# Optimization experiments

Measured on AMD Instinct MI355X. Metric: run time of the kernel, lower is better.

## Reference

```python
import jax, jax.numpy as jnp
import numpy as np

K_TOP = 4
NUM_EXPERTS = 8


def _lstm_dir(x, wih, whh, b):
    # x: [B,T,in], wih: [4H,in], whh: [4H,H], b: [4H] (b_ih+b_hh)
    xW = jnp.einsum('bti,gi->btg', x, wih) + b  # [B,T,4H]
    B = x.shape[0]
    H = whh.shape[1]
    init = (jnp.zeros((B, H), x.dtype), jnp.zeros((B, H), x.dtype))

    def step(carry, xt):
        h, c = carry
        g = xt + h @ whh.T
        i, f, gg, o = jnp.split(g, 4, axis=-1)  # torch gate order i,f,g,o
        c = jax.nn.sigmoid(f) * c + jax.nn.sigmoid(i) * jnp.tanh(gg)
        h = jax.nn.sigmoid(o) * jnp.tanh(c)
        return (h, c), h

    _, hs = jax.lax.scan(step, init, jnp.swapaxes(xW, 0, 1))  # [T,B,H]
    return jnp.swapaxes(hs, 0, 1)


def _bidir_layer(x, Wih, Whh, bih, bhh):
    # Wih: [2,4H,in]; dir 0 forward, dir 1 backward
    hf = _lstm_dir(x, Wih[0], Whh[0], bih[0] + bhh[0])
    hb = _lstm_dir(x[:, ::-1], Wih[1], Whh[1], bih[1] + bhh[1])[:, ::-1]
    return jnp.concatenate([hf, hb], axis=-1)  # [B,T,2H]


def _expert(x, Wih0, Whh0, bih0, bhh0, Wih1, Whh1, bih1, bhh1):
    h = _bidir_layer(x, Wih0, Whh0, bih0, bhh0)   # [B,T,2H]
    h = _bidir_layer(h, Wih1, Whh1, bih1, bhh1)   # [B,T,2H]
    return h


def _cv_squared(v):
    v = v.astype(jnp.float32)
    return jnp.var(v, ddof=1) / (jnp.mean(v) ** 2 + 1e-10)


def _forward(x, spk, wg_w, wg_b, Wih0, Whh0, bih0, bhh0, Wih1, Whh1, bih1, bhh1, fc1_w, fc1_b, fc_w, fc_b, loss_coef=0.01):
    B, T, _ = x.shape
    # --- top-k gating (eval path: clean logits, no noise) ---
    logits = spk @ wg_w.T + wg_b                      # [B,E]
    top_vals, top_idx = jax.lax.top_k(logits, K_TOP + 1)
    gates_k = jax.nn.softmax(top_vals[:, :K_TOP], axis=-1)
    rows = jnp.arange(B)[:, None]
    gates = jnp.zeros_like(logits).at[rows, top_idx[:, :K_TOP]].set(gates_k)  # [B,E]
    load = (gates > 0).sum(0)
    importance = gates.sum(0)
    loss = (_cv_squared(importance) + _cv_squared(load)) * loss_coef
    # --- run all experts (dense mixture, as in source) ---
    expert_h = jax.vmap(_expert, in_axes=(None, 0, 0, 0, 0, 0, 0, 0, 0))(
        x, Wih0, Whh0, bih0, bhh0, Wih1, Whh1, bih1, bhh1)          # [E,B,T,2H]
    expert_out = jnp.einsum('ebtf,hf->ebth', expert_h, fc1_w) + fc1_b  # [E,B,T,H]
    data_output = jnp.einsum('ebth,be->bth', expert_out, gates)        # [B,T,H]
    out = jnp.einsum('bth,oh->bto', data_output, fc_w) + fc_b          # [B,T,O]
    out = jnp.swapaxes(out, 0, 1)                                      # [T,B,O]
    return out, loss


def setup_inputs() -> dict:
    key = jax.random.key(0)
    ks = jax.random.split(key, 16)
    B, T, D, H, E, O, S = 32, 1024, 128, 128, 8, 44, 256
    s = 0.08  # weight scale to keep LSTM gates in sane range
    return {
        'x': jax.random.normal(ks[0], (B, T, D), jnp.float32),
        'spk': jax.random.normal(ks[1], (B, S), jnp.float32),
        'wg_w': jax.random.normal(ks[2], (E, S), jnp.float32) * s,
        'wg_b': jax.random.normal(ks[3], (E,), jnp.float32) * s,
        'Wih0': jax.random.normal(ks[4], (E, 2, 4 * H, D), jnp.float32) * s,
        'Whh0': jax.random.normal(ks[5], (E, 2, 4 * H, H), jnp.float32) * s,
        'bih0': jax.random.normal(ks[6], (E, 2, 4 * H), jnp.float32) * s,
        'bhh0': jax.random.normal(ks[7], (E, 2, 4 * H), jnp.float32) * s,
        'Wih1': jax.random.normal(ks[8], (E, 2, 4 * H, 2 * H), jnp.float32) * s,
        'Whh1': jax.random.normal(ks[9], (E, 2, 4 * H, H), jnp.float32) * s,
        'bih1': jax.random.normal(ks[10], (E, 2, 4 * H), jnp.float32) * s,
        'bhh1': jax.random.normal(ks[11], (E, 2, 4 * H), jnp.float32) * s,
        'fc1_w': jax.random.normal(ks[12], (H, 2 * H), jnp.float32) * s,
        'fc1_b': jax.random.normal(ks[13], (H,), jnp.float32) * s,
        'fc_w': jax.random.normal(ks[14], (O, H), jnp.float32) * s,
        'fc_b': jax.random.normal(ks[15], (O,), jnp.float32) * s,
    }


def reference(x, spk, wg_w, wg_b, Wih0, Whh0, bih0, bhh0, Wih1, Whh1, bih1, bhh1, fc1_w, fc1_b, fc_w, fc_b):
    return _forward(x, spk, wg_w, wg_b, Wih0, Whh0, bih0, bhh0, Wih1, Whh1, bih1, bhh1, fc1_w, fc1_b, fc_w, fc_b)
```

## Files before the change

### kernel.cpp

```cpp
#include <hip/hip_runtime.h>

typedef __attribute__((ext_vector_type(4))) float f32x4;
typedef __attribute__((ext_vector_type(8))) short s16x8;

#define LOG2E 1.4426950408889634f
#define K2L   2.8853900817779268f

__device__ __forceinline__ unsigned short f2bf(float f) {
  union { float f; unsigned int i; } v; v.f = f;
  unsigned int u = v.i;
  u = (u + 0x7FFFu + ((u >> 16) & 1u)) >> 16;
  return (unsigned short)u;
}
__device__ __forceinline__ float bf2f(unsigned short s) {
  union { unsigned int i; float f; } v; v.i = ((unsigned int)s) << 16;
  return v.f;
}
__device__ __forceinline__ float rcp_(float x) { return __builtin_amdgcn_rcpf(x); }
__device__ __forceinline__ float ex2(float x) { return __builtin_amdgcn_exp2f(x); }
__device__ __forceinline__ f32x4 mfma16(s16x8 a, s16x8 b, f32x4 c) {
  return __builtin_amdgcn_mfma_f32_16x16x32_bf16(a, b, c, 0, 0, 0);
}
__device__ __forceinline__ s16x8 pack8s(const float* s, float sc) {
  s16x8 v;
#pragma unroll
  for (int j = 0; j < 8; ++j) v[j] = (short)f2bf(s[j] * sc);
  return v;
}

#define OFF_H0   0
#define OFF_XW   134217728
#define OFF_XT   201326592
#define OFF_WHH  209715200
#define OFF_H1C  213909504
#define OFF_HST  230686720
#define OFF_CST  230817792
#define OFF_M    231079936
#define OFF_CV   231129088
#define OFF_G    231129344
#define OFF_WIH0 231130368
#define OFF_WIH1 233227520
#define OFF_BIA  237421824
#define WS_NEED  237552896

__global__ void wsdbg_kernel(float* __restrict__ out, float v) { out[0] = v; }

__global__ void prep_kernel(const float* __restrict__ Whh0, const float* __restrict__ Whh1,
                            const float* __restrict__ Wih0, const float* __restrict__ Wih1,
                            const float* __restrict__ bih0, const float* __restrict__ bhh0,
                            const float* __restrict__ bih1, const float* __restrict__ bhh1,
                            unsigned short* __restrict__ whhb,
                            unsigned short* __restrict__ wihb0,
                            unsigned short* __restrict__ wihb1,
                            float* __restrict__ biasb) {
  const int tid = blockIdx.x * 512 + threadIdx.x;
  for (int i = tid; i < 5242880; i += 2097152) {
    if (i < 2097152) {
      const int gate = (i >> 14) & 3;
      const float sc = (gate == 2) ? K2L : -LOG2E;
      whhb[i] = f2bf((i < 1048576 ? Whh0[i] : Whh1[i - 1048576]) * sc);
    } else if (i < 3145728) {
      const int j = i - 2097152;
      const int gate = (j >> 14) & 3;
      const float sc = (gate == 2) ? K2L : -LOG2E;
      wihb0[j] = f2bf(Wih0[j] * sc);
    } else {
      const int j = i - 3145728;
      const int gate = (j >> 15) & 3;
      const float sc = (gate == 2) ? K2L : -LOG2E;
      wihb1[j] = f2bf(Wih1[j] * sc);
    }
  }
  if (tid < 16384) {
    const int L = tid >> 13, rem = tid & 8191;
    const int gate = (rem >> 7) & 3;
    const float sc = (gate == 2) ? K2L : -LOG2E;
    const float b = L ? (bih1[rem] + bhh1[rem]) : (bih0[rem] + bhh0[rem]);
    biasb[tid] = b * sc;
  }
}

__global__ void prepx_kernel(const float* __restrict__ x, unsigned short* __restrict__ xt) {
  const int i = blockIdx.x * 512 + threadIdx.x;
  for (int j = i; j < 4194304; j += 2097152) {
    const int b = j >> 17, rem = j & 131071, t = rem >> 7, f = rem & 127;
    xt[((size_t)t * 32 + b) * 128 + f] = f2bf(x[j]);
  }
}

__global__ void mprep_kernel(const float* __restrict__ fc1w, const float* __restrict__ fc1b,
                             const float* __restrict__ fcw, const float* __restrict__ fcb,
                             float* __restrict__ M, float* __restrict__ Cv) {
  const int mi = blockIdx.x * 256 + threadIdx.x;
  if (mi < 12288) {
    const int dd = mi / 6144, rem = mi % 6144, o = rem >> 7, hc = rem & 127;
    float s = 0.f;
    if (o < 44)
      for (int h = 0; h < 128; ++h) s += fcw[o * 128 + h] * fc1w[h * 256 + dd * 128 + hc];
    M[mi] = s;
  }
  if (blockIdx.x == 0 && threadIdx.x < 44) {
    const int o = threadIdx.x;
    float s = fcb[o];
    for (int h = 0; h < 128; ++h) s += fcw[o * 128 + h] * fc1b[h];
    Cv[o] = s;
  }
}

__global__ void initout_kernel(const float* __restrict__ Cv, float* __restrict__ out) {
  const int i = blockIdx.x * 512 + threadIdx.x;
  if (i < 1441792) out[i] = Cv[i % 44];
}

__global__ void gating_kernel(const float* __restrict__ spk,
                              const float* __restrict__ wgw,
                              const float* __restrict__ wgb,
                              float* __restrict__ gates_out,
                              float* __restrict__ loss_out) {
  __shared__ __align__(16) float logits[32][8];
  __shared__ __align__(16) float gmat[32][8];
  const int tid = threadIdx.x;
  {
    const int b = tid >> 3, e = tid & 7;
    float s = wgb[e];
    for (int k = 0; k < 256; ++k) s += spk[b * 256 + k] * wgw[e * 256 + k];
    logits[b][e] = s;
  }
  __syncthreads();
  if (tid < 32) {
    const int b = tid;
    float v[8];
    for (int e = 0; e < 8; ++e) v[e] = logits[b][e];
    int idx[4]; float val[4];
    unsigned used = 0;
    for (int k = 0; k < 4; ++k) {
      float best = -1e30f; int bi = 0;
      for (int e = 0; e < 8; ++e)
        if (!((used >> e) & 1) && v[e] > best) { best = v[e]; bi = e; }
      used |= (1u << bi); idx[k] = bi; val[k] = best;
    }
    const float m = val[0];
    float ex[4], ssum = 0.f;
    for (int k = 0; k < 4; ++k) { ex[k] = ex2(LOG2E * (val[k] - m)); ssum += ex[k]; }
    for (int e = 0; e < 8; ++e) gmat[b][e] = 0.f;
    for (int k = 0; k < 4; ++k) gmat[b][idx[k]] = ex[k] / ssum;
    for (int e = 0; e < 8; ++e) gates_out[b * 8 + e] = gmat[b][e];
  }
  __syncthreads();
  if (tid == 0) {
    float imp[8], ld[8];
    for (int e = 0; e < 8; ++e) {
      float si = 0.f, sl = 0.f;
      for (int b = 0; b < 32; ++b) { si += gmat[b][e]; sl += (gmat[b][e] > 0.f) ? 1.f : 0.f; }
      imp[e] = si; ld[e] = sl;
    }
    float mi = 0.f, ml = 0.f;
    for (int e = 0; e < 8; ++e) { mi += imp[e]; ml += ld[e]; }
    mi *= 0.125f; ml *= 0.125f;
    float vi = 0.f, vl = 0.f;
    for (int e = 0; e < 8; ++e) {
      vi += (imp[e] - mi) * (imp[e] - mi);
      vl += (ld[e] - ml) * (ld[e] - ml);
    }
    vi /= 7.f; vl /= 7.f;
    loss_out[0] = 0.01f * (vi / (mi * mi + 1e-10f) + vl / (ml * ml + 1e-10f));
  }
}

template <int L>
__global__ __launch_bounds__(512, 1) void fused(
    int k,
    const unsigned short* __restrict__ Asrc,
    const unsigned short* __restrict__ wihb,
    const float* __restrict__ biasb,
    const unsigned short* __restrict__ whhb,
    unsigned short* __restrict__ xwbufs,
    unsigned short* __restrict__ hstate, float* __restrict__ cstate,
    unsigned short* __restrict__ hout,
    const float* __restrict__ Mmat, const float* __restrict__ gatesp,
    float* __restrict__ outp) {
  constexpr int KC = L ? 8 : 4;
  constexpr int KS = KC * 32;
  const int tid = threadIdx.x, w = tid >> 6, l = tid & 63;
  const int l15 = l & 15, lq = l >> 4;

  if (L && blockIdx.x >= 192) {
    const int c2 = k - 2;
    if (c2 < 0 || c2 > 15) return;
    if (w >= 6) return;
    const int ss = blockIdx.x - 192;
    const int mt = (w >= 3) ? 1 : 0, ot = w - mt * 3;
    const int o = ot * 16 + l15;
    const bool ov = o < 44;
    s16x8 bfm[2][4];
#pragma unroll
    for (int dd = 0; dd < 2; ++dd)
#pragma unroll
      for (int kc = 0; kc < 4; ++kc) {
        if (ov) bfm[dd][kc] = pack8s(Mmat + ((size_t)dd * 48 + o) * 128 + kc * 32 + lq * 8, 1.f);
        else { s16x8 z = {0,0,0,0,0,0,0,0}; bfm[dd][kc] = z; }
      }
    const unsigned short* hb = hout + (size_t)(c2 & 1) * 4194304;
    f32x4 acc0 = {0.f,0.f,0.f,0.f}, acc1 = {0.f,0.f,0.f,0.f};
    for (int e = 0; e < 8; ++e) {
      const unsigned short* ap = hb + ((((size_t)e * 64 + ss) * 32) + mt * 16 + l15) * 256 + lq * 8;
      f32x4 p0 = {0.f,0.f,0.f,0.f}, p1 = {0.f,0.f,0.f,0.f};
#pragma unroll
      for (int kc = 0; kc < 4; ++kc) {
        s16x8 a0 = *(const s16x8*)(ap + kc * 32);
        s16x8 a1 = *(const s16x8*)(ap + 128 + kc * 32);
        p0 = mfma16(a0, bfm[0][kc], p0);
        p1 = mfma16(a1, bfm[1][kc], p1);
      }
#pragma unroll
      for (int r = 0; r < 4; ++r) {
        const float g = gatesp[(mt * 16 + lq * 4 + r) * 8 + e];
        acc0[r] += g * p0[r];
        acc1[r] += g * p1[r];
      }
    }
    if (ov) {
      const int s2 = c2 * 64 + ss, t1 = 1023 - s2;
#pragma unroll
      for (int r = 0; r < 4; ++r) {
        const int b = mt * 16 + lq * 4 + r;
        outp[((size_t)s2 * 32 + b) * 44 + o] += acc0[r];
        outp[((size_t)t1 * 32 + b) * 44 + o] += acc1[r];
      }
    }
    return;
  }

  if (blockIdx.x >= 32) {
    if (k >= 16) return;
    const int gb = blockIdx.x - 32;
    const int ed = gb & 15, e = ed >> 1, d = ed & 1;
    const int slice = gb >> 4;
    const int nsl = L ? 10 : 14;
    unsigned short* xw = xwbufs + (size_t)(k & 1) * 16777216;

    s16x8 bf[4][KC];
    float bias[4];
#pragma unroll
    for (int j = 0; j < 4; ++j) {
      const int n = w * 64 + j * 16 + l15;
      bias[j] = biasb[ed * 512 + n];
      const unsigned short* wp = wihb + ((size_t)ed * 512 + n) * KS + lq * 8;
#pragma unroll
      for (int kc = 0; kc < KC; ++kc) bf[j][kc] = *(const s16x8*)(wp + kc * 32);
    }
    for (int ss = slice; ss < 64; ss += nsl) {
      const int s = k * 64 + ss;
      const int t = d ? 1023 - s : s;
#pragma unroll
      for (int mt = 0; mt < 2; ++mt) {
        const size_t arow = (size_t)(L ? (e * 1024 + t) : t) * 32 + mt * 16 + l15;
        const unsigned short* ap = Asrc + arow * KS + lq * 8;
        s16x8 af[KC];
#pragma unroll
        for (int kc = 0; kc < KC; ++kc) af[kc] = *(const s16x8*)(ap + kc * 32);
        f32x4 acc[4];
#pragma unroll
        for (int j = 0; j < 4; ++j) acc[j] = f32x4{bias[j], bias[j], bias[j], bias[j]};
#pragma unroll
        for (int kc = 0; kc < KC; ++kc) {
#pragma unroll
          for (int j = 0; j < 4; ++j) acc[j] = mfma16(af[kc], bf[j][kc], acc[j]);
        }
        unsigned short* op = xw + (((size_t)(ed * 2 + mt) * 64 + ss) * 512) * 16 + lq * 4;
#pragma unroll
        for (int j = 0; j < 4; ++j) {
          const int n = w * 64 + j * 16 + l15;
          ushort4 o4;
          o4.x = f2bf(acc[j][0]); o4.y = f2bf(acc[j][1]);
          o4.z = f2bf(acc[j][2]); o4.w = f2bf(acc[j][3]);
          *(ushort4*)(op + (size_t)n * 16) = o4;
        }
      }
    }
    return;
  }

  const int c = k - 1;
  if (c < 0 || c > 15) return;
  __builtin_amdgcn_s_setprio(2);
  const int rb = blockIdx.x, ed2 = rb >> 1, bh = rb & 1;
  const int e = ed2 >> 1, d = ed2 & 1;
  __shared__ __align__(16) char hbf[2][4096];
  const int cell = w * 16 + l15;

  s16x8 bfh[4][4];
#pragma unroll
  for (int g = 0; g < 4; ++g) {
    const unsigned short* wp = whhb + ((size_t)ed2 * 512 + g * 128 + cell) * 128 + lq * 8;
#pragma unroll
    for (int kc = 0; kc < 4; ++kc) bfh[g][kc] = *(const s16x8*)(wp + kc * 32);
  }
  const int wb0 = ((cell >> 5) << 10) | (((cell >> 3) & 3) << 8) | ((cell & 7) << 1);
  float cst[4];
  unsigned short hb4[4];
  if (c == 0) {
#pragma unroll
    for (int r = 0; r < 4; ++r) { cst[r] = 0.f; hb4[r] = 0; }
    if (tid < 256) {
      s16x8 z = {0,0,0,0,0,0,0,0};
      *(s16x8*)(&hbf[0][tid * 16]) = z;
    }
  } else {
    const float* cp = cstate + ((size_t)rb * 512 + tid) * 4;
    const unsigned short* hp = hstate + ((size_t)rb * 512 + tid) * 4;
#pragma unroll
    for (int r = 0; r < 4; ++r) {
      cst[r] = cp[r];
      hb4[r] = hp[r];
      *(unsigned short*)(&hbf[0][wb0 | ((lq * 4 + r) << 4)]) = hp[r];
    }
  }
  __syncthreads();

  const unsigned short* xwb =
      xwbufs + (size_t)(c & 1) * 16777216 + ((size_t)(ed2 * 2 + bh) * 64) * 8192 + cell * 16 + lq * 4;
  const int brow = bh * 16 + lq * 4;

  ushort4 xq[4];
#pragma unroll
  for (int g = 0; g < 4; ++g) xq[g] = *(const ushort4*)(xwb + g * 2048);

  for (int tt = 0; tt < 64; ++tt) {
    const int p = tt & 1;
    ushort4 nxq[4];
    {
      const int tn = tt < 63 ? tt + 1 : 63;
#pragma unroll
      for (int g = 0; g < 4; ++g) nxq[g] = *(const ushort4*)(xwb + (size_t)tn * 8192 + g * 2048);
    }
    if (tt > 0) {
      const int ptt = tt - 1;
      size_t ob;
      if (L) {
        ob = (size_t)(c & 1) * 4194304 + (((size_t)e * 64 + ptt) * 32 + brow) * 256 + d * 128 + cell;
      } else {
        const int s = c * 64 + ptt;
        const int tg = d ? 1023 - s : s;
        ob = (((size_t)e * 1024 + tg) * 32 + brow) * 256 + d * 128 + cell;
      }
#pragma unroll
      for (int r = 0; r < 4; ++r) hout[ob + (size_t)r * 256] = hb4[r];
    }

    s16x8 hf[4];
#pragma unroll
    for (int kc = 0; kc < 4; ++kc) hf[kc] = *(const s16x8*)(&hbf[p][kc * 1024 + l * 16]);
    f32x4 a[4];
#pragma unroll
    for (int g = 0; g < 4; ++g) {
      a[g][0] = bf2f(xq[g].x); a[g][1] = bf2f(xq[g].y);
      a[g][2] = bf2f(xq[g].z); a[g][3] = bf2f(xq[g].w);
    }
#pragma unroll
    for (int kc = 0; kc < 4; ++kc) {
#pragma unroll
      for (int g = 0; g < 4; ++g) a[g] = mfma16(hf[kc], bfh[g][kc], a[g]);
    }

#pragma unroll
    for (int r = 0; r < 4; ++r) {
      const float ai = ex2(a[0][r]);
      const float af = ex2(a[1][r]);
      const float bg = ex2(fminf(a[2][r], 80.f));
      const float ao = ex2(a[3][r]);
      const float sf = rcp_(1.f + af);
      const float r1 = rcp_((1.f + ai) * (1.f + bg));
      const float bgm = __builtin_fmaf(bg, K2L, -K2L);
      const float cc = __builtin_fmaf(sf, cst[r], bgm * r1);
      cst[r] = cc;
      const float qc = ex2(fminf(cc, 80.f));
      const float r2 = rcp_((1.f + ao) * (1.f + qc));
      hb4[r] = f2bf((qc - 1.f) * r2);
    }
    char* hw = &hbf[1 - p][0];
#pragma unroll
    for (int r = 0; r < 4; ++r)
      *(unsigned short*)(hw + (wb0 | ((lq * 4 + r) << 4))) = hb4[r];
    __syncthreads();
#pragma unroll
    for (int g = 0; g < 4; ++g) xq[g] = nxq[g];
  }

  {
    size_t ob;
    if (L) {
      ob = (size_t)(c & 1) * 4194304 + (((size_t)e * 64 + 63) * 32 + brow) * 256 + d * 128 + cell;
    } else {
      const int s = c * 64 + 63;
      const int tg = d ? 1023 - s : s;
      ob = (((size_t)e * 1024 + tg) * 32 + brow) * 256 + d * 128 + cell;
    }
#pragma unroll
    for (int r = 0; r < 4; ++r) hout[ob + (size_t)r * 256] = hb4[r];
    unsigned short* hsp = hstate + ((size_t)rb * 512 + tid) * 4;
    float* csp = cstate + ((size_t)rb * 512 + tid) * 4;
#pragma unroll
    for (int r = 0; r < 4; ++r) { hsp[r] = hb4[r]; csp[r] = cst[r]; }
  }
  __builtin_amdgcn_s_setprio(0);
}

extern "C" void kernel_launch(void* const* d_in, const int* in_sizes, int n_in,
                              void* d_out, int out_size, void* d_ws, size_t ws_size,
                              hipStream_t stream) {
  const float* x    = (const float*)d_in[0];
  const float* spk  = (const float*)d_in[1];
  const float* wgw  = (const float*)d_in[2];
  const float* wgb  = (const float*)d_in[3];
  const float* Wih0 = (const float*)d_in[4];
  const float* Whh0 = (const float*)d_in[5];
  const float* bih0 = (const float*)d_in[6];
  const float* bhh0 = (const float*)d_in[7];
  const float* Wih1 = (const float*)d_in[8];
  const float* Whh1 = (const float*)d_in[9];
  const float* bih1 = (const float*)d_in[10];
  const float* bhh1 = (const float*)d_in[11];
  const float* fc1w = (const float*)d_in[12];
  const float* fc1b = (const float*)d_in[13];
  const float* fcw  = (const float*)d_in[14];
  const float* fcb  = (const float*)d_in[15];
  float* out = (float*)d_out;

  if (ws_size < (size_t)WS_NEED) {
    wsdbg_kernel<<<1, 1, 0, stream>>>(out, (float)(ws_size >> 20));
    return;
  }
  char* ws = (char*)d_ws;
  unsigned short* h0     = (unsigned short*)(ws + OFF_H0);
  unsigned short* xwbufs = (unsigned short*)(ws + OFF_XW);
  unsigned short* xt     = (unsigned short*)(ws + OFF_XT);
  unsigned short* whhb   = (unsigned short*)(ws + OFF_WHH);
  unsigned short* h1c    = (unsigned short*)(ws + OFF_H1C);
  unsigned short* hstate = (unsigned short*)(ws + OFF_HST);
  float*          cstate = (float*)(ws + OFF_CST);
  float*          Mmat   = (float*)(ws + OFF_M);
  float*          Cv     = (float*)(ws + OFF_CV);
  float*          gatesw = (float*)(ws + OFF_G);
  unsigned short* wihb0  = (unsigned short*)(ws + OFF_WIH0);
  unsigned short* wihb1  = (unsigned short*)(ws + OFF_WIH1);
  float*          biasb  = (float*)(ws + OFF_BIA);

  prep_kernel<<<4096, 512, 0, stream>>>(Whh0, Whh1, Wih0, Wih1, bih0, bhh0, bih1, bhh1,
                                        whhb, wihb0, wihb1, biasb);
  prepx_kernel<<<4096, 512, 0, stream>>>(x, xt);
  mprep_kernel<<<48, 256, 0, stream>>>(fc1w, fc1b, fcw, fcb, Mmat, Cv);
  initout_kernel<<<2816, 512, 0, stream>>>(Cv, out);
  gating_kernel<<<1, 256, 0, stream>>>(spk, wgw, wgb, gatesw, out + 1441792);

  for (int k = 0; k <= 16; ++k)
    fused<0><<<256, 512, 0, stream>>>(k, xt, wihb0, biasb, whhb, xwbufs,
                                      hstate, cstate, h0, nullptr, nullptr, out);
  for (int k = 0; k <= 17; ++k)
    fused<1><<<256, 512, 0, stream>>>(k, h0, wihb1, biasb + 8192, whhb + 1048576, xwbufs,
                                      hstate, cstate, h1c, Mmat, gatesw, out);
}
```

Before: 2.060 ms.

## Merge batch-half recurrence blocks into 1024-thread blocks and rebalance projection work

Recurrent blocks now hold both batch halves of an expert-direction as two 512-thread halves of a single 1024-thread block, each half with its own LDS h buffer. Grid sizes shrink from 256 to 128/160 blocks, and the input-projection and output blocks are reshaped so each wave does fewer output columns and covers more time slices. The aim is to cut the number of blocks and rebalance work across CUs. The cost is that the shared __syncthreads now spans both halves, coupling their step timing, and register pressure per thread may rise under the new launch bounds.

```diff
diff --git a/kernel.cpp b/kernel.cpp
--- a/kernel.cpp
+++ b/kernel.cpp
@@ -168,7 +168,7 @@
 }
 
 template <int L>
-__global__ __launch_bounds__(512, 1) void fused(
+__global__ __launch_bounds__(1024, 4) void fused(
     int k,
     const unsigned short* __restrict__ Asrc,
     const unsigned short* __restrict__ wihb,
@@ -181,15 +181,18 @@
     float* __restrict__ outp) {
   constexpr int KC = L ? 8 : 4;
   constexpr int KS = KC * 32;
+  __shared__ __align__(16) char hbf[2][2][4096];
   const int tid = threadIdx.x, w = tid >> 6, l = tid & 63;
   const int l15 = l & 15, lq = l >> 4;
 
-  if (L && blockIdx.x >= 192) {
+  if (L && blockIdx.x >= 128) {
     const int c2 = k - 2;
     if (c2 < 0 || c2 > 15) return;
-    if (w >= 6) return;
-    const int ss = blockIdx.x - 192;
-    const int mt = (w >= 3) ? 1 : 0, ot = w - mt * 3;
+    const int w8 = w & 7;
+    if (w8 >= 6) return;
+    const int fb = blockIdx.x - 128;
+    const int ss = fb * 2 + (w >> 3);
+    const int mt = (w8 >= 3) ? 1 : 0, ot = w8 - mt * 3;
     const int o = ot * 16 + l15;
     const bool ov = o < 44;
     s16x8 bfm[2][4];
@@ -231,25 +234,24 @@
     return;
   }
 
-  if (blockIdx.x >= 32) {
+  if (blockIdx.x >= 16) {
     if (k >= 16) return;
-    const int gb = blockIdx.x - 32;
+    const int gb = blockIdx.x - 16;
     const int ed = gb & 15, e = ed >> 1, d = ed & 1;
     const int slice = gb >> 4;
-    const int nsl = L ? 10 : 14;
     unsigned short* xw = xwbufs + (size_t)(k & 1) * 16777216;
 
-    s16x8 bf[4][KC];
-    float bias[4];
-#pragma unroll
-    for (int j = 0; j < 4; ++j) {
-      const int n = w * 64 + j * 16 + l15;
+    s16x8 bf[2][KC];
+    float bias[2];
+#pragma unroll
+    for (int j = 0; j < 2; ++j) {
+      const int n = w * 32 + j * 16 + l15;
       bias[j] = biasb[ed * 512 + n];
       const unsigned short* wp = wihb + ((size_t)ed * 512 + n) * KS + lq * 8;
 #pragma unroll
       for (int kc = 0; kc < KC; ++kc) bf[j][kc] = *(const s16x8*)(wp + kc * 32);
     }
-    for (int ss = slice; ss < 64; ss += nsl) {
+    for (int ss = slice; ss < 64; ss += 7) {
       const int s = k * 64 + ss;
       const int t = d ? 1023 - s : s;
 #pragma unroll
@@ -259,18 +261,18 @@
         s16x8 af[KC];
 #pragma unroll
         for (int kc = 0; kc < KC; ++kc) af[kc] = *(const s16x8*)(ap + kc * 32);
-        f32x4 acc[4];
-#pragma unroll
-        for (int j = 0; j < 4; ++j) acc[j] = f32x4{bias[j], bias[j], bias[j], bias[j]};
+        f32x4 acc[2];
+#pragma unroll
+        for (int j = 0; j < 2; ++j) acc[j] = f32x4{bias[j], bias[j], bias[j], bias[j]};
 #pragma unroll
         for (int kc = 0; kc < KC; ++kc) {
 #pragma unroll
-          for (int j = 0; j < 4; ++j) acc[j] = mfma16(af[kc], bf[j][kc], acc[j]);
+          for (int j = 0; j < 2; ++j) acc[j] = mfma16(af[kc], bf[j][kc], acc[j]);
         }
         unsigned short* op = xw + (((size_t)(ed * 2 + mt) * 64 + ss) * 512) * 16 + lq * 4;
 #pragma unroll
-        for (int j = 0; j < 4; ++j) {
-          const int n = w * 64 + j * 16 + l15;
+        for (int j = 0; j < 2; ++j) {
+          const int n = w * 32 + j * 16 + l15;
           ushort4 o4;
           o4.x = f2bf(acc[j][0]); o4.y = f2bf(acc[j][1]);
           o4.z = f2bf(acc[j][2]); o4.w = f2bf(acc[j][3]);
@@ -284,15 +286,19 @@
   const int c = k - 1;
   if (c < 0 || c > 15) return;
   __builtin_amdgcn_s_setprio(2);
-  const int rb = blockIdx.x, ed2 = rb >> 1, bh = rb & 1;
+  const int ed2 = blockIdx.x;
+  const int ch = tid >> 9;
+  const int t5 = tid & 511;
+  const int w5 = t5 >> 6, l5 = t5 & 63;
+  const int l15r = l5 & 15, lqr = l5 >> 4;
   const int e = ed2 >> 1, d = ed2 & 1;
-  __shared__ __align__(16) char hbf[2][4096];
-  const int cell = w * 16 + l15;
+  const int cell = w5 * 16 + l15r;
+  const int sidx = ed2 * 2 + ch;
 
   s16x8 bfh[4][4];
 #pragma unroll
   for (int g = 0; g < 4; ++g) {
-    const unsigned short* wp = whhb + ((size_t)ed2 * 512 + g * 128 + cell) * 128 + lq * 8;
+    const unsigned short* wp = whhb + ((size_t)ed2 * 512 + g * 128 + cell) * 128 + lqr * 8;
 #pragma unroll
     for (int kc = 0; kc < 4; ++kc) bfh[g][kc] = *(const s16x8*)(wp + kc * 32);
   }
@@ -302,25 +308,25 @@
   if (c == 0) {
 #pragma unroll
     for (int r = 0; r < 4; ++r) { cst[r] = 0.f; hb4[r] = 0; }
-    if (tid < 256) {
+    if (t5 < 256) {
       s16x8 z = {0,0,0,0,0,0,0,0};
-      *(s16x8*)(&hbf[0][tid * 16]) = z;
+      *(s16x8*)(&hbf[ch][0][t5 * 16]) = z;
     }
   } else {
-    const float* cp = cstate + ((size_t)rb * 512 + tid) * 4;
-    const unsigned short* hp = hstate + ((size_t)rb * 512 + tid) * 4;
+    const float* cp = cstate + ((size_t)sidx * 512 + t5) * 4;
+    const unsigned short* hp = hstate + ((size_t)sidx * 512 + t5) * 4;
 #pragma unroll
     for (int r = 0; r < 4; ++r) {
       cst[r] = cp[r];
       hb4[r] = hp[r];
-      *(unsigned short*)(&hbf[0][wb0 | ((lq * 4 + r) << 4)]) = hp[r];
+      *(unsigned short*)(&hbf[ch][0][wb0 | ((lqr * 4 + r) << 4)]) = hp[r];
     }
   }
   __syncthreads();
 
   const unsigned short* xwb =
-      xwbufs + (size_t)(c & 1) * 16777216 + ((size_t)(ed2 * 2 + bh) * 64) * 8192 + cell * 16 + lq * 4;
-  const int brow = bh * 16 + lq * 4;
+      xwbufs + (size_t)(c & 1) * 16777216 + ((size_t)(ed2 * 2 + ch) * 64) * 8192 + cell * 16 + lqr * 4;
+  const int brow = ch * 16 + lqr * 4;
 
   ushort4 xq[4];
 #pragma unroll
@@ -350,7 +356,7 @@
 
     s16x8 hf[4];
 #pragma unroll
-    for (int kc = 0; kc < 4; ++kc) hf[kc] = *(const s16x8*)(&hbf[p][kc * 1024 + l * 16]);
+    for (int kc = 0; kc < 4; ++kc) hf[kc] = *(const s16x8*)(&hbf[ch][p][kc * 1024 + l5 * 16]);
     f32x4 a[4];
 #pragma unroll
     for (int g = 0; g < 4; ++g) {
@@ -378,10 +384,10 @@
       const float r2 = rcp_((1.f + ao) * (1.f + qc));
       hb4[r] = f2bf((qc - 1.f) * r2);
     }
-    char* hw = &hbf[1 - p][0];
+    char* hw = &hbf[ch][1 - p][0];
 #pragma unroll
     for (int r = 0; r < 4; ++r)
-      *(unsigned short*)(hw + (wb0 | ((lq * 4 + r) << 4))) = hb4[r];
+      *(unsigned short*)(hw + (wb0 | ((lqr * 4 + r) << 4))) = hb4[r];
     __syncthreads();
 #pragma unroll
     for (int g = 0; g < 4; ++g) xq[g] = nxq[g];
@@ -398,8 +404,8 @@
     }
 #pragma unroll
     for (int r = 0; r < 4; ++r) hout[ob + (size_t)r * 256] = hb4[r];
-    unsigned short* hsp = hstate + ((size_t)rb * 512 + tid) * 4;
-    float* csp = cstate + ((size_t)rb * 512 + tid) * 4;
+    unsigned short* hsp = hstate + ((size_t)sidx * 512 + t5) * 4;
+    float* csp = cstate + ((size_t)sidx * 512 + t5) * 4;
 #pragma unroll
     for (int r = 0; r < 4; ++r) { hsp[r] = hb4[r]; csp[r] = cst[r]; }
   }
@@ -454,9 +460,9 @@
   gating_kernel<<<1, 256, 0, stream>>>(spk, wgw, wgb, gatesw, out + 1441792);
 
   for (int k = 0; k <= 16; ++k)
-    fused<0><<<256, 512, 0, stream>>>(k, xt, wihb0, biasb, whhb, xwbufs,
-                                      hstate, cstate, h0, nullptr, nullptr, out);
+    fused<0><<<128, 1024, 0, stream>>>(k, xt, wihb0, biasb, whhb, xwbufs,
+                                       hstate, cstate, h0, nullptr, nullptr, out);
   for (int k = 0; k <= 17; ++k)
-    fused<1><<<256, 512, 0, stream>>>(k, h0, wihb1, biasb + 8192, whhb + 1048576, xwbufs,
-                                      hstate, cstate, h1c, Mmat, gatesw, out);
-}
+    fused<1><<<160, 1024, 0, stream>>>(k, h0, wihb1, biasb + 8192, whhb + 1048576, xwbufs,
+                                       hstate, cstate, h1c, Mmat, gatesw, out);
+}
```

After: 3.443 ms. 1.67x slower.

## Transpose MFMA operands in LSTM recurrence for vectorized h stores and swizzled LDS

Applied to the files above, without the earlier changes.

Swaps the A/B operands of the MFMA in both the input-projection and recurrent kernels, so each lane now holds four consecutive hidden cells for one batch row instead of four batch rows for one cell. The xW buffer layout, the LDS hidden-state layout (now XOR-swizzled by row) and the output/state addressing are all changed to match, which allows ushort4 stores to global memory and LDS in place of scalar stores. The recurrent matmul is also split into two independent accumulator chains that are summed at the end, shortening the serial MFMA dependency on the per-timestep critical path. All producer and consumer indexing has to stay consistent, and a layout mismatch would silently corrupt results.

```diff
diff --git a/kernel.cpp b/kernel.cpp
--- a/kernel.cpp
+++ b/kernel.cpp
@@ -240,14 +240,14 @@
     unsigned short* xw = xwbufs + (size_t)(k & 1) * 16777216;
 
     s16x8 bf[4][KC];
-    float bias[4];
+    f32x4 bias4[4];
 #pragma unroll
     for (int j = 0; j < 4; ++j) {
       const int n = w * 64 + j * 16 + l15;
-      bias[j] = biasb[ed * 512 + n];
       const unsigned short* wp = wihb + ((size_t)ed * 512 + n) * KS + lq * 8;
 #pragma unroll
       for (int kc = 0; kc < KC; ++kc) bf[j][kc] = *(const s16x8*)(wp + kc * 32);
+      bias4[j] = *(const f32x4*)(biasb + ed * 512 + w * 64 + j * 16 + lq * 4);
     }
     for (int ss = slice; ss < 64; ss += nsl) {
       const int s = k * 64 + ss;
@@ -261,20 +261,19 @@
         for (int kc = 0; kc < KC; ++kc) af[kc] = *(const s16x8*)(ap + kc * 32);
         f32x4 acc[4];
 #pragma unroll
-        for (int j = 0; j < 4; ++j) acc[j] = f32x4{bias[j], bias[j], bias[j], bias[j]};
+        for (int j = 0; j < 4; ++j) acc[j] = bias4[j];
 #pragma unroll
         for (int kc = 0; kc < KC; ++kc) {
 #pragma unroll
-          for (int j = 0; j < 4; ++j) acc[j] = mfma16(af[kc], bf[j][kc], acc[j]);
+          for (int j = 0; j < 4; ++j) acc[j] = mfma16(bf[j][kc], af[kc], acc[j]);
         }
-        unsigned short* op = xw + (((size_t)(ed * 2 + mt) * 64 + ss) * 512) * 16 + lq * 4;
+        unsigned short* op = xw + (((size_t)(ed * 2 + mt) * 64 + ss) * 16 + l15) * 512 + w * 64 + lq * 4;
 #pragma unroll
         for (int j = 0; j < 4; ++j) {
-          const int n = w * 64 + j * 16 + l15;
           ushort4 o4;
           o4.x = f2bf(acc[j][0]); o4.y = f2bf(acc[j][1]);
           o4.z = f2bf(acc[j][2]); o4.w = f2bf(acc[j][3]);
-          *(ushort4*)(op + (size_t)n * 16) = o4;
+          *(ushort4*)(op + j * 16) = o4;
         }
       }
     }
@@ -287,21 +286,24 @@
   const int rb = blockIdx.x, ed2 = rb >> 1, bh = rb & 1;
   const int e = ed2 >> 1, d = ed2 & 1;
   __shared__ __align__(16) char hbf[2][4096];
-  const int cell = w * 16 + l15;
+  const int row = l15;
+  const int cellb = w * 16 + lq * 4;
 
   s16x8 bfh[4][4];
 #pragma unroll
   for (int g = 0; g < 4; ++g) {
-    const unsigned short* wp = whhb + ((size_t)ed2 * 512 + g * 128 + cell) * 128 + lq * 8;
+    const unsigned short* wp = whhb + ((size_t)ed2 * 512 + g * 128 + w * 16 + l15) * 128 + lq * 8;
 #pragma unroll
     for (int kc = 0; kc < 4; ++kc) bfh[g][kc] = *(const s16x8*)(wp + kc * 32);
   }
-  const int wb0 = ((cell >> 5) << 10) | (((cell >> 3) & 3) << 8) | ((cell & 7) << 1);
+  const int swz = (row & 7) << 4;
+  const int wbyte = row * 256 + ((w * 32 + lq * 8) ^ swz);
   float cst[4];
-  unsigned short hb4[4];
+  ushort4 hb4;
   if (c == 0) {
 #pragma unroll
-    for (int r = 0; r < 4; ++r) { cst[r] = 0.f; hb4[r] = 0; }
+    for (int r = 0; r < 4; ++r) cst[r] = 0.f;
+    hb4.x = 0; hb4.y = 0; hb4.z = 0; hb4.w = 0;
     if (tid < 256) {
       s16x8 z = {0,0,0,0,0,0,0,0};
       *(s16x8*)(&hbf[0][tid * 16]) = z;
@@ -310,21 +312,19 @@
     const float* cp = cstate + ((size_t)rb * 512 + tid) * 4;
     const unsigned short* hp = hstate + ((size_t)rb * 512 + tid) * 4;
 #pragma unroll
-    for (int r = 0; r < 4; ++r) {
-      cst[r] = cp[r];
-      hb4[r] = hp[r];
-      *(unsigned short*)(&hbf[0][wb0 | ((lq * 4 + r) << 4)]) = hp[r];
-    }
+    for (int r = 0; r < 4; ++r) cst[r] = cp[r];
+    hb4 = *(const ushort4*)hp;
+    *(ushort4*)(&hbf[0][wbyte]) = hb4;
   }
   __syncthreads();
 
-  const unsigned short* xwb =
-      xwbufs + (size_t)(c & 1) * 16777216 + ((size_t)(ed2 * 2 + bh) * 64) * 8192 + cell * 16 + lq * 4;
-  const int brow = bh * 16 + lq * 4;
+  const unsigned short* xwp =
+      xwbufs + (size_t)(c & 1) * 16777216 + ((size_t)(ed2 * 2 + bh) * 64) * 8192 + row * 512 + cellb;
+  const int grow = bh * 16 + row;
 
   ushort4 xq[4];
 #pragma unroll
-  for (int g = 0; g < 4; ++g) xq[g] = *(const ushort4*)(xwb + g * 2048);
+  for (int g = 0; g < 4; ++g) xq[g] = *(const ushort4*)(xwp + g * 128);
 
   for (int tt = 0; tt < 64; ++tt) {
     const int p = tt & 1;
@@ -332,43 +332,54 @@
     {
       const int tn = tt < 63 ? tt + 1 : 63;
 #pragma unroll
-      for (int g = 0; g < 4; ++g) nxq[g] = *(const ushort4*)(xwb + (size_t)tn * 8192 + g * 2048);
+      for (int g = 0; g < 4; ++g)
+        nxq[g] = *(const ushort4*)(xwp + (size_t)tn * 8192 + g * 128);
     }
     if (tt > 0) {
       const int ptt = tt - 1;
       size_t ob;
       if (L) {
-        ob = (size_t)(c & 1) * 4194304 + (((size_t)e * 64 + ptt) * 32 + brow) * 256 + d * 128 + cell;
+        ob = (size_t)(c & 1) * 4194304 + (((size_t)e * 64 + ptt) * 32 + grow) * 256 + d * 128 + cellb;
       } else {
         const int s = c * 64 + ptt;
         const int tg = d ? 1023 - s : s;
-        ob = (((size_t)e * 1024 + tg) * 32 + brow) * 256 + d * 128 + cell;
-      }
-#pragma unroll
-      for (int r = 0; r < 4; ++r) hout[ob + (size_t)r * 256] = hb4[r];
+        ob = (((size_t)e * 1024 + tg) * 32 + grow) * 256 + d * 128 + cellb;
+      }
+      *(ushort4*)(hout + ob) = hb4;
     }
 
     s16x8 hf[4];
 #pragma unroll
-    for (int kc = 0; kc < 4; ++kc) hf[kc] = *(const s16x8*)(&hbf[p][kc * 1024 + l * 16]);
-    f32x4 a[4];
+    for (int kc = 0; kc < 4; ++kc)
+      hf[kc] = *(const s16x8*)(&hbf[p][row * 256 + ((kc * 64 + lq * 16) ^ swz)]);
+
+    f32x4 aA[4], aB[4];
 #pragma unroll
     for (int g = 0; g < 4; ++g) {
-      a[g][0] = bf2f(xq[g].x); a[g][1] = bf2f(xq[g].y);
-      a[g][2] = bf2f(xq[g].z); a[g][3] = bf2f(xq[g].w);
-    }
-#pragma unroll
-    for (int kc = 0; kc < 4; ++kc) {
-#pragma unroll
-      for (int g = 0; g < 4; ++g) a[g] = mfma16(hf[kc], bfh[g][kc], a[g]);
-    }
-
+      aA[g][0] = bf2f(xq[g].x); aA[g][1] = bf2f(xq[g].y);
+      aA[g][2] = bf2f(xq[g].z); aA[g][3] = bf2f(xq[g].w);
+      aB[g] = f32x4{0.f, 0.f, 0.f, 0.f};
+    }
+#pragma unroll
+    for (int g = 0; g < 4; ++g) {
+      aA[g] = mfma16(bfh[g][0], hf[0], aA[g]);
+      aB[g] = mfma16(bfh[g][2], hf[2], aB[g]);
+    }
+#pragma unroll
+    for (int g = 0; g < 4; ++g) {
+      aA[g] = mfma16(bfh[g][1], hf[1], aA[g]);
+      aB[g] = mfma16(bfh[g][3], hf[3], aB[g]);
+    }
+#pragma unroll
+    for (int g = 0; g < 4; ++g) aA[g] += aB[g];
+
+    unsigned short hh[4];
 #pragma unroll
     for (int r = 0; r < 4; ++r) {
-      const float ai = ex2(a[0][r]);
-      const float af = ex2(a[1][r]);
-      const float bg = ex2(fminf(a[2][r], 80.f));
-      const float ao = ex2(a[3][r]);
+      const float ai = ex2(aA[0][r]);
+      const float af = ex2(aA[1][r]);
+      const float bg = ex2(fminf(aA[2][r], 80.f));
+      const float ao = ex2(aA[3][r]);
       const float sf = rcp_(1.f + af);
       const float r1 = rcp_((1.f + ai) * (1.f + bg));
       const float bgm = __builtin_fmaf(bg, K2L, -K2L);
@@ -376,12 +387,10 @@
       cst[r] = cc;
       const float qc = ex2(fminf(cc, 80.f));
       const float r2 = rcp_((1.f + ao) * (1.f + qc));
-      hb4[r] = f2bf((qc - 1.f) * r2);
-    }
-    char* hw = &hbf[1 - p][0];
-#pragma unroll
-    for (int r = 0; r < 4; ++r)
-      *(unsigned short*)(hw + (wb0 | ((lq * 4 + r) << 4))) = hb4[r];
+      hh[r] = f2bf((qc - 1.f) * r2);
+    }
+    hb4.x = hh[0]; hb4.y = hh[1]; hb4.z = hh[2]; hb4.w = hh[3];
+    *(ushort4*)(&hbf[1 - p][wbyte]) = hb4;
     __syncthreads();
 #pragma unroll
     for (int g = 0; g < 4; ++g) xq[g] = nxq[g];
@@ -390,18 +399,18 @@
   {
     size_t ob;
     if (L) {
-      ob = (size_t)(c & 1) * 4194304 + (((size_t)e * 64 + 63) * 32 + brow) * 256 + d * 128 + cell;
+      ob = (size_t)(c & 1) * 4194304 + (((size_t)e * 64 + 63) * 32 + grow) * 256 + d * 128 + cellb;
     } else {
       const int s = c * 64 + 63;
       const int tg = d ? 1023 - s : s;
-      ob = (((size_t)e * 1024 + tg) * 32 + brow) * 256 + d * 128 + cell;
-    }
-#pragma unroll
-    for (int r = 0; r < 4; ++r) hout[ob + (size_t)r * 256] = hb4[r];
+      ob = (((size_t)e * 1024 + tg) * 32 + grow) * 256 + d * 128 + cellb;
+    }
+    *(ushort4*)(hout + ob) = hb4;
     unsigned short* hsp = hstate + ((size_t)rb * 512 + tid) * 4;
     float* csp = cstate + ((size_t)rb * 512 + tid) * 4;
-#pragma unroll
-    for (int r = 0; r < 4; ++r) { hsp[r] = hb4[r]; csp[r] = cst[r]; }
+    *(ushort4*)hsp = hb4;
+#pragma unroll
+    for (int r = 0; r < 4; ++r) csp[r] = cst[r];
   }
   __builtin_amdgcn_s_setprio(0);
 }
```

New measurement: 2.246 ms. +9.0%, slower.
